# Kernel tuning notes

Measured on AMD Instinct MI355X. Metric: run time of the kernel, lower is better.

Reference implementation:

```python
import jax, jax.numpy as jnp
import numpy as np

N_NODES = 50000
N_EDGES = 600000
IN_DIM = 128
OUT_DIM = 128
N_REL = 32
N_BASES = 4
BN_EPS = 1e-5


def setup_inputs() -> dict:
    key = jax.random.key(0)
    ks = jax.random.split(key, 8)
    entity_emb = jax.random.normal(ks[0], (N_NODES, IN_DIM), dtype=jnp.float32)
    bases = jax.random.normal(ks[1], (N_BASES, IN_DIM, OUT_DIM), dtype=jnp.float32) * 0.05
    coefficients = jax.random.normal(ks[2], (N_REL, N_BASES), dtype=jnp.float32) * 0.5
    W_loop = jax.random.normal(ks[3], (IN_DIM, OUT_DIM), dtype=jnp.float32) * 0.05
    b_loop = jnp.zeros((OUT_DIM,), dtype=jnp.float32)
    gamma = jnp.ones((OUT_DIM,), dtype=jnp.float32)
    beta = jnp.zeros((OUT_DIM,), dtype=jnp.float32)
    edge_index = jax.random.randint(ks[4], (2, N_EDGES), 0, N_NODES, dtype=jnp.int32)
    edge_type = jax.random.randint(ks[5], (N_EDGES,), 0, N_REL, dtype=jnp.int32)
    return {"entity_emb": entity_emb, "bases": bases, "coefficients": coefficients,
            "W_loop": W_loop, "b_loop": b_loop, "gamma": gamma, "beta": beta,
            "edge_index": edge_index, "edge_type": edge_type}


def reference(entity_emb, bases, coefficients, W_loop, b_loop, gamma, beta, edge_index, edge_type):
    N = entity_emb.shape[0]
    # self-loop linear
    out = entity_emb @ W_loop + b_loop  # [N, out_dim]
    # basis decomposition: per-relation weight W[r] = sum_b coeff[r,b] * bases[b]
    W = jnp.einsum('rb,bio->rio', coefficients, bases)  # [R, in, out]
    src, dst = edge_index[0], edge_index[1]
    # per-edge message: entity_emb[src_e] @ W[edge_type_e]  (vectorizes the per-relation loop)
    msg = jnp.einsum('ei,eio->eo', entity_emb[src], W[edge_type])  # [E, out]
    out = out + jax.ops.segment_sum(msg, dst, num_segments=N)
    # degree normalization (in-degree over all edges, clamped at 1)
    deg = jax.ops.segment_sum(jnp.ones_like(dst, dtype=out.dtype), dst, num_segments=N)
    out = out / jnp.maximum(deg, 1.0)[:, None]
    # BatchNorm1d (training mode: biased batch stats over node dim)
    mean = jnp.mean(out, axis=0)
    var = jnp.mean((out - mean) ** 2, axis=0)
    out = (out - mean) / jnp.sqrt(var + BN_EPS) * gamma + beta
    return jax.nn.relu(out)
```

## Files before the change

### kernel.cpp

```cpp
#include <hip/hip_runtime.h>
#include <cstdint>

#define NN 50000
#define NE 600000
#define NPAIRS 1563
#define GSTRIDE 512

typedef unsigned short ushort_t;
typedef __bf16 bf16_t;
typedef __attribute__((ext_vector_type(8))) bf16_t bf16x8;
typedef __attribute__((ext_vector_type(8))) ushort_t ushort8;
typedef __attribute__((ext_vector_type(4))) float f32x4;
typedef __attribute__((ext_vector_type(2))) float f32x2;

#define WT_OFF   0ul
#define XGG_OFF  40960ul
#define XBF_OFF  12845056ul
#define CNT_OFF  16046080ul
#define CUR_OFF  16096080ul
#define BSUM_OFF 16146080ul
#define BSCN_OFF 16146208ul
#define CS_OFF   16146336ul
#define CSQ_OFF  16146464ul

__device__ __forceinline__ float2 bf2_to_f2(uint32_t u) {
    float2 r;
    r.x = __uint_as_float(u << 16);
    r.y = __uint_as_float(u & 0xffff0000u);
    return r;
}

__device__ __forceinline__ ushort_t f2bf(float f) {
    uint32_t u = __float_as_uint(f);
    u = (u + 0x7fffu + ((u >> 16) & 1u)) >> 16;
    return (ushort_t)u;
}

__device__ __forceinline__ uint32_t f2bf2(float x, float y) {
    return (uint32_t)f2bf(x) | ((uint32_t)f2bf(y) << 16);
}

__device__ __forceinline__ void async_copy16(const void* g, void* l) {
    __builtin_amdgcn_global_load_lds(
        (const __attribute__((address_space(1))) void*)g,
        (__attribute__((address_space(3))) void*)l, 16, 0, 0);
}

__global__ __launch_bounds__(256) void k_pre(
    const float* __restrict__ X, const float* __restrict__ Wl,
    const float* __restrict__ bases, const int* __restrict__ eidx,
    ushort_t* __restrict__ WT, ushort_t* __restrict__ Xbf,
    int* __restrict__ cnt)
{
    const int b = blockIdx.x;
    const int tid = threadIdx.x;
    if (b < 320) {
        const int i = b * 256 + tid;
        const int n = i / 640;
        const int kk = i - n * 640;
        float v;
        if (kk < 128) v = Wl[kk * 128 + n];
        else {
            const int j = kk - 128;
            v = bases[(size_t)(j >> 7) * 16384 + (j & 127) * 128 + n];
        }
        WT[i] = f2bf(v);
    } else if (b < 3445) {
        const int tile = b - 320;
        const int row = tid >> 4, gc = tid & 15;
        const int node = tile * 16 + row;
        const float4* p = (const float4*)(X + (size_t)node * 128 + gc * 8);
        const float4 a = p[0], c = p[1];
        ushort_t t8[8] = { f2bf(a.x), f2bf(a.y), f2bf(a.z), f2bf(a.w),
                           f2bf(c.x), f2bf(c.y), f2bf(c.z), f2bf(c.w) };
        *(uint4*)(Xbf + (size_t)node * 128 + gc * 8) = *(const uint4*)t8;
    } else {
        const int* __restrict__ dst = eidx + NE;
        for (int e = (b - 3445) * 256 + tid; e < NE; e += 2048 * 256)
            atomicAdd(cnt + dst[e], 1);
    }
}

__global__ __launch_bounds__(256) void k_scan1(
    const int* __restrict__ cnt, int* __restrict__ curs, int* __restrict__ bsum)
{
    __shared__ int sh[256];
    const int tid = threadIdx.x;
    const int i0 = blockIdx.x * 512 + tid * 2;
    const int v0 = (i0 < NN) ? cnt[i0] : 0;
    const int v1 = (i0 + 1 < NN) ? cnt[i0 + 1] : 0;
    int s = v0 + v1;
    sh[tid] = s;
    __syncthreads();
#pragma unroll
    for (int off = 1; off < 256; off <<= 1) {
        int t = (tid >= off) ? sh[tid - off] : 0;
        __syncthreads();
        sh[tid] += t;
        __syncthreads();
    }
    const int excl = sh[tid] - s;
    if (i0 < NN) curs[i0] = excl;
    if (i0 + 1 < NN) curs[i0 + 1] = excl + v0;
    if (tid == 255) bsum[blockIdx.x] = sh[255];
}

__global__ __launch_bounds__(128) void k_scan2(
    const int* __restrict__ bsum, int* __restrict__ bscan, int nblk)
{
    __shared__ int sh[128];
    const int tid = threadIdx.x;
    int v = (tid < nblk) ? bsum[tid] : 0;
    sh[tid] = v;
    __syncthreads();
#pragma unroll
    for (int off = 1; off < 128; off <<= 1) {
        int t = (tid >= off) ? sh[tid - off] : 0;
        __syncthreads();
        sh[tid] += t;
        __syncthreads();
    }
    if (tid < nblk) bscan[tid] = sh[tid] - v;
}

__global__ __launch_bounds__(256) void k_scan3(
    int* __restrict__ curs, const int* __restrict__ bscan)
{
    const int add = bscan[blockIdx.x];
    const int i0 = blockIdx.x * 512 + threadIdx.x * 2;
    if (i0 < NN) curs[i0] += add;
    if (i0 + 1 < NN) curs[i0 + 1] += add;
}

__global__ __launch_bounds__(256) void k_scatter(
    const int* __restrict__ eidx, const int* __restrict__ etype,
    int* __restrict__ curs, uint32_t* __restrict__ epack)
{
    const int* __restrict__ src = eidx;
    const int* __restrict__ dst = eidx + NE;
    for (int e = blockIdx.x * 256 + threadIdx.x; e < NE; e += gridDim.x * 256) {
        const int d = dst[e];
        const int pos = atomicAdd(curs + d, 1);
        epack[pos] = (uint32_t)src[e] | ((uint32_t)etype[e] << 16);
    }
}

__device__ __forceinline__ void accum_pk(
    const uint4 xv, const float4 cw, f32x2* m2)
{
    f32x2 x2[4];
    float2 p;
    p = bf2_to_f2(xv.x); x2[0] = f32x2{p.x, p.y};
    p = bf2_to_f2(xv.y); x2[1] = f32x2{p.x, p.y};
    p = bf2_to_f2(xv.z); x2[2] = f32x2{p.x, p.y};
    p = bf2_to_f2(xv.w); x2[3] = f32x2{p.x, p.y};
#pragma unroll
    for (int c2 = 0; c2 < 4; ++c2) {
        m2[0 * 4 + c2] += cw.x * x2[c2];
        m2[1 * 4 + c2] += cw.y * x2[c2];
        m2[2 * 4 + c2] += cw.z * x2[c2];
        m2[3 * 4 + c2] += cw.w * x2[c2];
    }
}

__global__ __launch_bounds__(256, 4) void k_gather(
    const ushort_t* __restrict__ Xbf, const uint32_t* __restrict__ epack,
    const int* __restrict__ cnt, const int* __restrict__ curs,
    const float* __restrict__ coeff, ushort_t* __restrict__ XG_G)
{
    const int lane = threadIdx.x & 63;
    const int w = threadIdx.x >> 6;
    const int sub = lane >> 4;
    const int k = lane & 15;
    const int tile = blockIdx.x;
    const int d = tile * 16 + w * 4 + sub;

    const int n = cnt[d];
    const int end = curs[d];
    int j = end - n;

    f32x2 m2[16];
#pragma unroll
    for (int i = 0; i < 16; ++i) m2[i] = f32x2{0.f, 0.f};

    for (; j + 7 < end; j += 8) {
        uint32_t ep[8];
#pragma unroll
        for (int i = 0; i < 8; ++i) ep[i] = epack[j + i];
        uint4 xv[8];
        float4 cw[8];
#pragma unroll
        for (int i = 0; i < 8; ++i) {
            const int s = ep[i] & 0xffff;
            const int t = ep[i] >> 16;
            xv[i] = *(const uint4*)(Xbf + (size_t)s * 128 + k * 8);
            cw[i] = *(const float4*)(coeff + t * 4);
        }
#pragma unroll
        for (int i = 0; i < 8; ++i) accum_pk(xv[i], cw[i], m2);
    }
    if (j + 3 < end) {
        uint32_t ep[4];
#pragma unroll
        for (int i = 0; i < 4; ++i) ep[i] = epack[j + i];
        uint4 xv[4];
        float4 cw[4];
#pragma unroll
        for (int i = 0; i < 4; ++i) {
            const int s = ep[i] & 0xffff;
            const int t = ep[i] >> 16;
            xv[i] = *(const uint4*)(Xbf + (size_t)s * 128 + k * 8);
            cw[i] = *(const float4*)(coeff + t * 4);
        }
#pragma unroll
        for (int i = 0; i < 4; ++i) accum_pk(xv[i], cw[i], m2);
        j += 4;
    }
    for (; j < end; ++j) {
        const uint32_t ep = epack[j];
        const int s = ep & 0xffff;
        const int t = ep >> 16;
        const uint4 xv = *(const uint4*)(Xbf + (size_t)s * 128 + k * 8);
        const float4 cw = *(const float4*)(coeff + t * 4);
        accum_pk(xv, cw, m2);
    }

    uint32_t* gb = (uint32_t*)(XG_G + (size_t)tile * 8192);
#pragma unroll
    for (int b = 0; b < 4; ++b) {
        uint4 v;
        v.x = f2bf2(m2[b * 4 + 0][0], m2[b * 4 + 0][1]);
        v.y = f2bf2(m2[b * 4 + 1][0], m2[b * 4 + 1][1]);
        v.z = f2bf2(m2[b * 4 + 2][0], m2[b * 4 + 2][1]);
        v.w = f2bf2(m2[b * 4 + 3][0], m2[b * 4 + 3][1]);
        *(uint4*)(gb + (b * 16 + k) * 64 + (w * 4 + sub) * 4) = v;
    }
}

__global__ __launch_bounds__(256, 2) void k_gemm_f(
    const ushort_t* __restrict__ XG_G, const ushort_t* __restrict__ WT,
    const ushort_t* __restrict__ Xbf, const float* __restrict__ bl,
    const int* __restrict__ cnt, float* __restrict__ out,
    float* __restrict__ colsum, float* __restrict__ colsq)
{
    __shared__ ushort_t As[2][2][10240];
    const int tid = threadIdx.x;
    const int lane = tid & 63;
    const int w = tid >> 6;
    const int m = lane & 15;
    const int quad = lane >> 4;

    auto stage = [&](int buf, int pr) {
#pragma unroll
        for (int j = 0; j < 10; ++j) {
            const int idx = w * 10 + j;
            const int tl = idx / 20;
            const int off = idx - tl * 20;
            const int tile = pr * 2 + tl;
            const ushort_t* src;
            if (off < 4) {
                const int node = tile * 16 + (lane & 15);
                const int g = off * 4 + (lane >> 4);
                src = Xbf + (size_t)node * 128 + g * 8;
            } else {
                src = XG_G + (size_t)tile * 8192 + (off - 4) * 512 + lane * 8;
            }
            async_copy16(src, &As[buf][tl][off * 512]);
        }
    };

    int p = blockIdx.x;
    stage(0, p);

    const ushort_t* bp0 = WT + (size_t)(w * 32 + m) * 640 + quad * 8;
    const ushort_t* bp1 = bp0 + 16 * 640;
    ushort8 B0[20], B1[20];
#pragma unroll
    for (int c = 0; c < 20; ++c) {
        B0[c] = *(const ushort8*)(bp0 + c * 32);
        B1[c] = *(const ushort8*)(bp1 + c * 32);
    }
    const float blv0 = bl[w * 32 + m];
    const float blv1 = bl[w * 32 + 16 + m];
    float s0 = 0.f, q0 = 0.f, s1 = 0.f, q1 = 0.f;

    __syncthreads();

    int buf = 0;
    while (p < NPAIRS) {
        const int pn = p + GSTRIDE;
        if (pn < NPAIRS) stage(buf ^ 1, pn);

        f32x4 cc[2][2];
#pragma unroll
        for (int rt = 0; rt < 2; ++rt)
#pragma unroll
            for (int ct = 0; ct < 2; ++ct)
#pragma unroll
                for (int i = 0; i < 4; ++i) cc[rt][ct][i] = 0.f;

#pragma unroll
        for (int c = 0; c < 20; ++c) {
            const int aoff = (c * 4 + quad) * 128 + m * 8;
            const bf16x8 a0 = __builtin_bit_cast(bf16x8, *(const ushort8*)&As[buf][0][aoff]);
            const bf16x8 a1 = __builtin_bit_cast(bf16x8, *(const ushort8*)&As[buf][1][aoff]);
            const bf16x8 b0 = __builtin_bit_cast(bf16x8, B0[c]);
            const bf16x8 b1 = __builtin_bit_cast(bf16x8, B1[c]);
            cc[0][0] = __builtin_amdgcn_mfma_f32_16x16x32_bf16(a0, b0, cc[0][0], 0, 0, 0);
            cc[0][1] = __builtin_amdgcn_mfma_f32_16x16x32_bf16(a0, b1, cc[0][1], 0, 0, 0);
            cc[1][0] = __builtin_amdgcn_mfma_f32_16x16x32_bf16(a1, b0, cc[1][0], 0, 0, 0);
            cc[1][1] = __builtin_amdgcn_mfma_f32_16x16x32_bf16(a1, b1, cc[1][1], 0, 0, 0);
        }

        const int row0 = p * 32;
#pragma unroll
        for (int rt = 0; rt < 2; ++rt) {
            const int rowb = row0 + rt * 16 + quad * 4;
#pragma unroll
            for (int r = 0; r < 4; ++r) {
                const int row = rowb + r;
                if (row < NN) {
                    const int dg = cnt[row];
                    const float inv = 1.0f / (float)((dg > 0) ? dg : 1);
                    float* po = out + (size_t)row * 128 + w * 32 + m;
                    const float v0 = (cc[rt][0][r] + blv0) * inv;
                    const float v1 = (cc[rt][1][r] + blv1) * inv;
                    po[0]  = v0;
                    po[16] = v1;
                    s0 += v0; q0 += v0 * v0;
                    s1 += v1; q1 += v1 * v1;
                }
            }
        }

        if (pn < NPAIRS) __syncthreads();
        buf ^= 1;
        p = pn;
    }

    s0 += __shfl_down(s0, 32); q0 += __shfl_down(q0, 32);
    s0 += __shfl_down(s0, 16); q0 += __shfl_down(q0, 16);
    s1 += __shfl_down(s1, 32); q1 += __shfl_down(q1, 32);
    s1 += __shfl_down(s1, 16); q1 += __shfl_down(q1, 16);
    if (lane < 16) {
        atomicAdd(colsum + w * 32 + lane, s0);
        atomicAdd(colsq  + w * 32 + lane, q0);
        atomicAdd(colsum + w * 32 + 16 + lane, s1);
        atomicAdd(colsq  + w * 32 + 16 + lane, q1);
    }
}

__global__ __launch_bounds__(256) void k_bn_relu(
    float* __restrict__ out, const float* __restrict__ colsum,
    const float* __restrict__ colsq, const float* __restrict__ gamma,
    const float* __restrict__ beta)
{
    __shared__ float sc[128], sh[128];
    const int tid = threadIdx.x;
    if (tid < 128) {
        const float mean = colsum[tid] * (1.0f / NN);
        const float var = colsq[tid] * (1.0f / NN) - mean * mean;
        const float g = gamma[tid] * rsqrtf(var + 1e-5f);
        sc[tid] = g;
        sh[tid] = beta[tid] - mean * g;
    }
    __syncthreads();
    const int total = NN * 32;
    for (int i = blockIdx.x * 256 + tid; i < total; i += gridDim.x * 256) {
        const int c = (i & 31) << 2;
        float4 v = *(float4*)(out + (size_t)i * 4);
        v.x = fmaxf(fmaf(v.x, sc[c + 0], sh[c + 0]), 0.f);
        v.y = fmaxf(fmaf(v.y, sc[c + 1], sh[c + 1]), 0.f);
        v.z = fmaxf(fmaf(v.z, sc[c + 2], sh[c + 2]), 0.f);
        v.w = fmaxf(fmaf(v.w, sc[c + 3], sh[c + 3]), 0.f);
        *(float4*)(out + (size_t)i * 4) = v;
    }
}

extern "C" void kernel_launch(void* const* d_in, const int* in_sizes, int n_in,
                              void* d_out, int out_size, void* d_ws, size_t ws_size,
                              hipStream_t stream)
{
    const float* X      = (const float*)d_in[0];
    const float* bases  = (const float*)d_in[1];
    const float* coeff  = (const float*)d_in[2];
    const float* Wl     = (const float*)d_in[3];
    const float* bl     = (const float*)d_in[4];
    const float* gamma  = (const float*)d_in[5];
    const float* beta   = (const float*)d_in[6];
    const int*   eidx   = (const int*)d_in[7];
    const int*   etype  = (const int*)d_in[8];
    float* out = (float*)d_out;

    float* ws = (float*)d_ws;
    ushort_t* WT     = (ushort_t*)(ws + WT_OFF);
    ushort_t* XG_G   = (ushort_t*)(ws + XGG_OFF);
    ushort_t* Xbf    = (ushort_t*)(ws + XBF_OFF);
    int*      cnt    = (int*)(ws + CNT_OFF);
    int*      curs   = (int*)(ws + CUR_OFF);
    int*      bsum   = (int*)(ws + BSUM_OFF);
    int*      bscan  = (int*)(ws + BSCN_OFF);
    float*    colsum = ws + CS_OFF;
    float*    colsq  = ws + CSQ_OFF;
    uint32_t* epack  = (uint32_t*)d_out;

    hipMemsetAsync(cnt, 0, (CSQ_OFF + 128 - CNT_OFF) * sizeof(float), stream);

    const int nblk_scan = (NN + 511) / 512;

    k_pre<<<5493, 256, 0, stream>>>(X, Wl, bases, eidx, WT, Xbf, cnt);
    k_scan1<<<nblk_scan, 256, 0, stream>>>(cnt, curs, bsum);
    k_scan2<<<1, 128, 0, stream>>>(bsum, bscan, nblk_scan);
    k_scan3<<<nblk_scan, 256, 0, stream>>>(curs, bscan);
    k_scatter<<<2048, 256, 0, stream>>>(eidx, etype, curs, epack);
    k_gather<<<3125, 256, 0, stream>>>(Xbf, epack, cnt, curs, coeff, XG_G);
    k_gemm_f<<<GSTRIDE, 256, 0, stream>>>(XG_G, WT, Xbf, bl, cnt,
                                          out, colsum, colsq);
    k_bn_relu<<<1024, 256, 0, stream>>>(out, colsum, colsq, gamma, beta);
}
```

Baseline: 243.9 us.

## Fuse gather-aggregation with MFMA projection and shard column-stat atomics

Result: slower. 263.3 us (+8.0%).

```diff
diff --git a/kernel.cpp b/kernel.cpp
--- a/kernel.cpp
+++ b/kernel.cpp
@@ -3,8 +3,6 @@
 
 #define NN 50000
 #define NE 600000
-#define NPAIRS 1563
-#define GSTRIDE 512
 
 typedef unsigned short ushort_t;
 typedef __bf16 bf16_t;
@@ -14,14 +12,14 @@
 typedef __attribute__((ext_vector_type(2))) float f32x2;
 
 #define WT_OFF   0ul
-#define XGG_OFF  40960ul
-#define XBF_OFF  12845056ul
-#define CNT_OFF  16046080ul
-#define CUR_OFF  16096080ul
-#define BSUM_OFF 16146080ul
-#define BSCN_OFF 16146208ul
-#define CS_OFF   16146336ul
-#define CSQ_OFF  16146464ul
+#define XBF_OFF  40960ul
+#define EPK_OFF  3240960ul
+#define CNT_OFF  3840960ul
+#define CUR_OFF  3890960ul
+#define BSUM_OFF 3940960ul
+#define BSCN_OFF 3941088ul
+#define CSS_OFF  3941216ul
+#define CSQS_OFF 3945312ul
 
 __device__ __forceinline__ float2 bf2_to_f2(uint32_t u) {
     float2 r;
@@ -163,18 +161,29 @@
     }
 }
 
-__global__ __launch_bounds__(256, 4) void k_gather(
+__global__ __launch_bounds__(256, 4) void k_gather_mm(
     const ushort_t* __restrict__ Xbf, const uint32_t* __restrict__ epack,
     const int* __restrict__ cnt, const int* __restrict__ curs,
-    const float* __restrict__ coeff, ushort_t* __restrict__ XG_G)
-{
-    const int lane = threadIdx.x & 63;
-    const int w = threadIdx.x >> 6;
-    const int sub = lane >> 4;
-    const int k = lane & 15;
+    const float* __restrict__ coeff, const ushort_t* __restrict__ WT,
+    const float* __restrict__ bl, float* __restrict__ out,
+    float* __restrict__ colsum_s, float* __restrict__ colsq_s)
+{
+    __shared__ ushort_t A[10240];
+    const int tid = threadIdx.x;
+    const int lane = tid & 63;
+    const int w = tid >> 6;
+    const int m = lane & 15;
+    const int quad = lane >> 4;
     const int tile = blockIdx.x;
-    const int d = tile * 16 + w * 4 + sub;
-
+
+    {
+        const int g = w * 4 + quad;
+        const int r = m ^ g;
+        const ushort_t* src = Xbf + (size_t)(tile * 16 + r) * 128 + g * 8;
+        async_copy16(src, &A[(size_t)w * 512 + lane * 8]);
+    }
+
+    const int d = tile * 16 + w * 4 + quad;
     const int n = cnt[d];
     const int end = curs[d];
     int j = end - n;
@@ -193,7 +202,7 @@
         for (int i = 0; i < 8; ++i) {
             const int s = ep[i] & 0xffff;
             const int t = ep[i] >> 16;
-            xv[i] = *(const uint4*)(Xbf + (size_t)s * 128 + k * 8);
+            xv[i] = *(const uint4*)(Xbf + (size_t)s * 128 + m * 8);
             cw[i] = *(const float4*)(coeff + t * 4);
         }
 #pragma unroll
@@ -209,7 +218,7 @@
         for (int i = 0; i < 4; ++i) {
             const int s = ep[i] & 0xffff;
             const int t = ep[i] >> 16;
-            xv[i] = *(const uint4*)(Xbf + (size_t)s * 128 + k * 8);
+            xv[i] = *(const uint4*)(Xbf + (size_t)s * 128 + m * 8);
             cw[i] = *(const float4*)(coeff + t * 4);
         }
 #pragma unroll
@@ -220,122 +229,62 @@
         const uint32_t ep = epack[j];
         const int s = ep & 0xffff;
         const int t = ep >> 16;
-        const uint4 xv = *(const uint4*)(Xbf + (size_t)s * 128 + k * 8);
+        const uint4 xv = *(const uint4*)(Xbf + (size_t)s * 128 + m * 8);
         const float4 cw = *(const float4*)(coeff + t * 4);
         accum_pk(xv, cw, m2);
     }
 
-    uint32_t* gb = (uint32_t*)(XG_G + (size_t)tile * 8192);
-#pragma unroll
-    for (int b = 0; b < 4; ++b) {
-        uint4 v;
-        v.x = f2bf2(m2[b * 4 + 0][0], m2[b * 4 + 0][1]);
-        v.y = f2bf2(m2[b * 4 + 1][0], m2[b * 4 + 1][1]);
-        v.z = f2bf2(m2[b * 4 + 2][0], m2[b * 4 + 2][1]);
-        v.w = f2bf2(m2[b * 4 + 3][0], m2[b * 4 + 3][1]);
-        *(uint4*)(gb + (b * 16 + k) * 64 + (w * 4 + sub) * 4) = v;
-    }
-}
-
-__global__ __launch_bounds__(256, 2) void k_gemm_f(
-    const ushort_t* __restrict__ XG_G, const ushort_t* __restrict__ WT,
-    const ushort_t* __restrict__ Xbf, const float* __restrict__ bl,
-    const int* __restrict__ cnt, float* __restrict__ out,
-    float* __restrict__ colsum, float* __restrict__ colsq)
-{
-    __shared__ ushort_t As[2][2][10240];
-    const int tid = threadIdx.x;
-    const int lane = tid & 63;
-    const int w = tid >> 6;
-    const int m = lane & 15;
-    const int quad = lane >> 4;
-
-    auto stage = [&](int buf, int pr) {
-#pragma unroll
-        for (int j = 0; j < 10; ++j) {
-            const int idx = w * 10 + j;
-            const int tl = idx / 20;
-            const int off = idx - tl * 20;
-            const int tile = pr * 2 + tl;
-            const ushort_t* src;
-            if (off < 4) {
-                const int node = tile * 16 + (lane & 15);
-                const int g = off * 4 + (lane >> 4);
-                src = Xbf + (size_t)node * 128 + g * 8;
-            } else {
-                src = XG_G + (size_t)tile * 8192 + (off - 4) * 512 + lane * 8;
-            }
-            async_copy16(src, &As[buf][tl][off * 512]);
-        }
-    };
-
-    int p = blockIdx.x;
-    stage(0, p);
+    {
+        const int r = w * 4 + quad;
+#pragma unroll
+        for (int b = 0; b < 4; ++b) {
+            const int g = 16 + b * 16 + m;
+            uint4 v;
+            v.x = f2bf2(m2[b * 4 + 0][0], m2[b * 4 + 0][1]);
+            v.y = f2bf2(m2[b * 4 + 1][0], m2[b * 4 + 1][1]);
+            v.z = f2bf2(m2[b * 4 + 2][0], m2[b * 4 + 2][1]);
+            v.w = f2bf2(m2[b * 4 + 3][0], m2[b * 4 + 3][1]);
+            *(uint4*)&A[(size_t)g * 128 + (size_t)((r ^ m)) * 8] = v;
+        }
+    }
+
+    __syncthreads();
 
     const ushort_t* bp0 = WT + (size_t)(w * 32 + m) * 640 + quad * 8;
     const ushort_t* bp1 = bp0 + 16 * 640;
-    ushort8 B0[20], B1[20];
+    f32x4 cc[2];
+#pragma unroll
+    for (int ct = 0; ct < 2; ++ct)
+#pragma unroll
+        for (int i = 0; i < 4; ++i) cc[ct][i] = 0.f;
+
 #pragma unroll
     for (int c = 0; c < 20; ++c) {
-        B0[c] = *(const ushort8*)(bp0 + c * 32);
-        B1[c] = *(const ushort8*)(bp1 + c * 32);
-    }
+        const int g = c * 4 + quad;
+        const int aoff = g * 128 + ((m ^ (g & 15)) * 8);
+        const bf16x8 a  = __builtin_bit_cast(bf16x8, *(const ushort8*)&A[aoff]);
+        const bf16x8 b0 = __builtin_bit_cast(bf16x8, *(const ushort8*)(bp0 + c * 32));
+        const bf16x8 b1 = __builtin_bit_cast(bf16x8, *(const ushort8*)(bp1 + c * 32));
+        cc[0] = __builtin_amdgcn_mfma_f32_16x16x32_bf16(a, b0, cc[0], 0, 0, 0);
+        cc[1] = __builtin_amdgcn_mfma_f32_16x16x32_bf16(a, b1, cc[1], 0, 0, 0);
+    }
+
     const float blv0 = bl[w * 32 + m];
     const float blv1 = bl[w * 32 + 16 + m];
     float s0 = 0.f, q0 = 0.f, s1 = 0.f, q1 = 0.f;
-
-    __syncthreads();
-
-    int buf = 0;
-    while (p < NPAIRS) {
-        const int pn = p + GSTRIDE;
-        if (pn < NPAIRS) stage(buf ^ 1, pn);
-
-        f32x4 cc[2][2];
-#pragma unroll
-        for (int rt = 0; rt < 2; ++rt)
-#pragma unroll
-            for (int ct = 0; ct < 2; ++ct)
-#pragma unroll
-                for (int i = 0; i < 4; ++i) cc[rt][ct][i] = 0.f;
-
-#pragma unroll
-        for (int c = 0; c < 20; ++c) {
-            const int aoff = (c * 4 + quad) * 128 + m * 8;
-            const bf16x8 a0 = __builtin_bit_cast(bf16x8, *(const ushort8*)&As[buf][0][aoff]);
-            const bf16x8 a1 = __builtin_bit_cast(bf16x8, *(const ushort8*)&As[buf][1][aoff]);
-            const bf16x8 b0 = __builtin_bit_cast(bf16x8, B0[c]);
-            const bf16x8 b1 = __builtin_bit_cast(bf16x8, B1[c]);
-            cc[0][0] = __builtin_amdgcn_mfma_f32_16x16x32_bf16(a0, b0, cc[0][0], 0, 0, 0);
-            cc[0][1] = __builtin_amdgcn_mfma_f32_16x16x32_bf16(a0, b1, cc[0][1], 0, 0, 0);
-            cc[1][0] = __builtin_amdgcn_mfma_f32_16x16x32_bf16(a1, b0, cc[1][0], 0, 0, 0);
-            cc[1][1] = __builtin_amdgcn_mfma_f32_16x16x32_bf16(a1, b1, cc[1][1], 0, 0, 0);
-        }
-
-        const int row0 = p * 32;
-#pragma unroll
-        for (int rt = 0; rt < 2; ++rt) {
-            const int rowb = row0 + rt * 16 + quad * 4;
-#pragma unroll
-            for (int r = 0; r < 4; ++r) {
-                const int row = rowb + r;
-                if (row < NN) {
-                    const int dg = cnt[row];
-                    const float inv = 1.0f / (float)((dg > 0) ? dg : 1);
-                    float* po = out + (size_t)row * 128 + w * 32 + m;
-                    const float v0 = (cc[rt][0][r] + blv0) * inv;
-                    const float v1 = (cc[rt][1][r] + blv1) * inv;
-                    po[0]  = v0;
-                    po[16] = v1;
-                    s0 += v0; q0 += v0 * v0;
-                    s1 += v1; q1 += v1 * v1;
-                }
-            }
-        }
-
-        if (pn < NPAIRS) __syncthreads();
-        buf ^= 1;
-        p = pn;
+    const int rowb = tile * 16 + quad * 4;
+#pragma unroll
+    for (int r = 0; r < 4; ++r) {
+        const int row = rowb + r;
+        const int dg = cnt[row];
+        const float inv = 1.0f / (float)((dg > 0) ? dg : 1);
+        float* po = out + (size_t)row * 128 + w * 32 + m;
+        const float v0 = (cc[0][r] + blv0) * inv;
+        const float v1 = (cc[1][r] + blv1) * inv;
+        po[0]  = v0;
+        po[16] = v1;
+        s0 += v0; q0 += v0 * v0;
+        s1 += v1; q1 += v1 * v1;
     }
 
     s0 += __shfl_down(s0, 32); q0 += __shfl_down(q0, 32);
@@ -343,23 +292,30 @@
     s1 += __shfl_down(s1, 32); q1 += __shfl_down(q1, 32);
     s1 += __shfl_down(s1, 16); q1 += __shfl_down(q1, 16);
     if (lane < 16) {
-        atomicAdd(colsum + w * 32 + lane, s0);
-        atomicAdd(colsq  + w * 32 + lane, q0);
-        atomicAdd(colsum + w * 32 + 16 + lane, s1);
-        atomicAdd(colsq  + w * 32 + 16 + lane, q1);
+        const int sl = (blockIdx.x & 31) * 128;
+        atomicAdd(colsum_s + sl + w * 32 + lane, s0);
+        atomicAdd(colsq_s  + sl + w * 32 + lane, q0);
+        atomicAdd(colsum_s + sl + w * 32 + 16 + lane, s1);
+        atomicAdd(colsq_s  + sl + w * 32 + 16 + lane, q1);
     }
 }
 
 __global__ __launch_bounds__(256) void k_bn_relu(
-    float* __restrict__ out, const float* __restrict__ colsum,
-    const float* __restrict__ colsq, const float* __restrict__ gamma,
+    float* __restrict__ out, const float* __restrict__ colsum_s,
+    const float* __restrict__ colsq_s, const float* __restrict__ gamma,
     const float* __restrict__ beta)
 {
     __shared__ float sc[128], sh[128];
     const int tid = threadIdx.x;
     if (tid < 128) {
-        const float mean = colsum[tid] * (1.0f / NN);
-        const float var = colsq[tid] * (1.0f / NN) - mean * mean;
+        float cs = 0.f, cq = 0.f;
+#pragma unroll
+        for (int s = 0; s < 32; ++s) {
+            cs += colsum_s[s * 128 + tid];
+            cq += colsq_s[s * 128 + tid];
+        }
+        const float mean = cs * (1.0f / NN);
+        const float var = cq * (1.0f / NN) - mean * mean;
         const float g = gamma[tid] * rsqrtf(var + 1e-5f);
         sc[tid] = g;
         sh[tid] = beta[tid] - mean * g;
@@ -393,18 +349,17 @@
     float* out = (float*)d_out;
 
     float* ws = (float*)d_ws;
-    ushort_t* WT     = (ushort_t*)(ws + WT_OFF);
-    ushort_t* XG_G   = (ushort_t*)(ws + XGG_OFF);
-    ushort_t* Xbf    = (ushort_t*)(ws + XBF_OFF);
-    int*      cnt    = (int*)(ws + CNT_OFF);
-    int*      curs   = (int*)(ws + CUR_OFF);
-    int*      bsum   = (int*)(ws + BSUM_OFF);
-    int*      bscan  = (int*)(ws + BSCN_OFF);
-    float*    colsum = ws + CS_OFF;
-    float*    colsq  = ws + CSQ_OFF;
-    uint32_t* epack  = (uint32_t*)d_out;
-
-    hipMemsetAsync(cnt, 0, (CSQ_OFF + 128 - CNT_OFF) * sizeof(float), stream);
+    ushort_t* WT       = (ushort_t*)(ws + WT_OFF);
+    ushort_t* Xbf      = (ushort_t*)(ws + XBF_OFF);
+    uint32_t* epack    = (uint32_t*)(ws + EPK_OFF);
+    int*      cnt      = (int*)(ws + CNT_OFF);
+    int*      curs     = (int*)(ws + CUR_OFF);
+    int*      bsum     = (int*)(ws + BSUM_OFF);
+    int*      bscan    = (int*)(ws + BSCN_OFF);
+    float*    colsum_s = ws + CSS_OFF;
+    float*    colsq_s  = ws + CSQS_OFF;
+
+    hipMemsetAsync(cnt, 0, (CSQS_OFF + 4096 - CNT_OFF) * sizeof(float), stream);
 
     const int nblk_scan = (NN + 511) / 512;
 
@@ -413,8 +368,7 @@
     k_scan2<<<1, 128, 0, stream>>>(bsum, bscan, nblk_scan);
     k_scan3<<<nblk_scan, 256, 0, stream>>>(curs, bscan);
     k_scatter<<<2048, 256, 0, stream>>>(eidx, etype, curs, epack);
-    k_gather<<<3125, 256, 0, stream>>>(Xbf, epack, cnt, curs, coeff, XG_G);
-    k_gemm_f<<<GSTRIDE, 256, 0, stream>>>(XG_G, WT, Xbf, bl, cnt,
-                                          out, colsum, colsq);
-    k_bn_relu<<<1024, 256, 0, stream>>>(out, colsum, colsq, gamma, beta);
-}
+    k_gather_mm<<<3125, 256, 0, stream>>>(Xbf, epack, cnt, curs, coeff,
+                                          WT, bl, out, colsum_s, colsq_s);
+    k_bn_relu<<<1024, 256, 0, stream>>>(out, colsum_s, colsq_s, gamma, beta);
+}
```
